# Optimization experiments

Hardware: AMD Instinct MI355X
Metric: run time of the kernel (lower is better)

## Reference

```python
import jax, jax.numpy as jnp
import numpy as np

IN_F, OUT_F = 1024, 1024
GRID_SIZE, SPLINE_ORDER = 5, 3
BATCH = 4096


def _make_grid():
    # grid_range = [-1, 1], h = 2 / grid_size
    h = 2.0 / GRID_SIZE
    g = jnp.arange(-SPLINE_ORDER, GRID_SIZE + SPLINE_ORDER + 1, dtype=jnp.float32) * h - 1.0
    return jnp.broadcast_to(g, (IN_F, g.shape[0]))  # [in, 12]


def setup_inputs() -> dict:
    key = jax.random.key(0)
    k1, k2, k3, k4 = jax.random.split(key, 4)
    x = jax.random.normal(k1, (BATCH, IN_F), dtype=jnp.float32) * 0.5
    base_weight = jax.random.normal(k2, (OUT_F, IN_F), dtype=jnp.float32) * (1.0 / np.sqrt(IN_F))
    # matches reset_parameters noise scale: (rand-0.5)*0.1/grid_size
    spline_weight = (jax.random.uniform(k3, (OUT_F, IN_F, GRID_SIZE + SPLINE_ORDER)) - 0.5) * (0.1 / GRID_SIZE)
    spline_scaler = jax.random.normal(k4, (OUT_F, IN_F), dtype=jnp.float32) * (1.0 / np.sqrt(IN_F))
    return {"x": x, "base_weight": base_weight, "spline_weight": spline_weight,
            "spline_scaler": spline_scaler, "grid": _make_grid()}


def _b_splines(x, grid):
    # x: [B, F], grid: [F, G]; returns [B, F, grid_size + spline_order]
    xe = x[..., None]  # [B, F, 1]
    bases = ((xe >= grid[:, :-1]) & (xe < grid[:, 1:])).astype(x.dtype)  # [B,F,G-1]
    for k in range(1, SPLINE_ORDER + 1):
        left = (xe - grid[:, : -(k + 1)]) / (grid[:, k:-1] - grid[:, : -(k + 1)])
        right = (grid[:, k + 1 :] - xe) / (grid[:, k + 1 :] - grid[:, 1:-k])
        bases = left * bases[:, :, :-1] + right * bases[:, :, 1:]
    return bases


def reference(x, base_weight, spline_weight, spline_scaler, grid):
    base_out = jax.nn.silu(x) @ base_weight.T  # [B, out]
    basis = _b_splines(x, grid)  # [B, in, 8]
    scaled_w = spline_weight * spline_scaler[..., None]  # [out, in, 8]
    spline_out = jnp.einsum('bfi,ofi->bo', basis, scaled_w)
    return base_out + spline_out
```

## Files before the change

### kernel.cpp

```cpp
#include <hip/hip_runtime.h>
#include <hip/hip_bf16.h>

#define IN_F   1024
#define OUT_F  1024
#define GS     5
#define SO     3
#define NB     (GS + SO)
#define NG     (GS + 2*SO + 1)
#define BATCH  4096
#define KC     (IN_F + IN_F * NB)
#define BM 128
#define BN 128
#define BK 64
#define SPLITK 2
#define KPART  (KC / SPLITK)
#define NT     (KPART / BK)

typedef __bf16 bf16x8 __attribute__((ext_vector_type(8)));
typedef float  f32x4  __attribute__((ext_vector_type(4)));

__device__ __forceinline__ void gload_lds16(const void* g, void* l) {
    __builtin_amdgcn_global_load_lds(
        (const __attribute__((address_space(1))) void*)g,
        (__attribute__((address_space(3))) void*)l,
        16, 0, 0);
}

#define WC_BLK 4608
#define A_BLK  18432

__global__ __launch_bounds__(256) void prep_all(const float* __restrict__ bw,
                                                const float* __restrict__ sw,
                                                const float* __restrict__ ss,
                                                const float* __restrict__ x,
                                                __bf16* __restrict__ W,
                                                __bf16* __restrict__ A) {
    if (blockIdx.x < WC_BLK) {
        const int t = blockIdx.x * 256 + threadIdx.x;
        const int NBASE = OUT_F * IN_F / 8;
        if (t < NBASE) {
            const int o  = t >> 7;
            const int c8 = (t & 127) * 8;
            const float4* sp = (const float4*)(bw + (size_t)o * IN_F + c8);
            float4 v0 = sp[0], v1 = sp[1];
            float v[8] = {v0.x, v0.y, v0.z, v0.w, v1.x, v1.y, v1.z, v1.w};
            bf16x8 ov;
#pragma unroll
            for (int j = 0; j < 8; ++j) ov[j] = (__bf16)v[j];
            *(bf16x8*)(W + (size_t)o * KC + c8) = ov;
        } else {
            const int u = t - NBASE;
            if (u >= OUT_F * IN_F) return;
            const int o = u >> 10, f = u & 1023;
            const float s = ss[(size_t)o * IN_F + f];
            const float4* sp = (const float4*)(sw + ((size_t)o * IN_F + f) * NB);
            float4 v0 = sp[0], v1 = sp[1];
            float v[8] = {v0.x, v0.y, v0.z, v0.w, v1.x, v1.y, v1.z, v1.w};
            bf16x8 ov;
#pragma unroll
            for (int j = 0; j < 8; ++j) ov[j] = (__bf16)(v[j] * s);
            *(bf16x8*)(W + (size_t)o * KC + IN_F + (size_t)f * NB) = ov;
        }
    } else {
        const int t = (blockIdx.x - WC_BLK) * 256 + threadIdx.x;
        const int NBASE = BATCH * IN_F / 8;
        if (t < NBASE) {
            const int b  = t >> 7;
            const int c8 = (t & 127) * 8;
            const float4* sp = (const float4*)(x + (size_t)b * IN_F + c8);
            float4 v0 = sp[0], v1 = sp[1];
            float v[8] = {v0.x, v0.y, v0.z, v0.w, v1.x, v1.y, v1.z, v1.w};
            bf16x8 ov;
#pragma unroll
            for (int j = 0; j < 8; ++j) {
                float xx = v[j];
                ov[j] = (__bf16)(xx / (1.0f + __expf(-xx)));
            }
            *(bf16x8*)(A + (size_t)b * KC + c8) = ov;
        } else {
            const int u = t - NBASE;
            if (u >= BATCH * IN_F) return;
            const int b = u >> 10, f = u & 1023;
            const float xv = x[(size_t)b * IN_F + f];
            const float h = 2.0f / GS;
            float gv[NG];
#pragma unroll
            for (int j = 0; j < NG; ++j) gv[j] = (float)(j - SO) * h - 1.0f;
            float bas[NB + SO];
#pragma unroll
            for (int j = 0; j < NB + SO; ++j)
                bas[j] = (xv >= gv[j] && xv < gv[j + 1]) ? 1.0f : 0.0f;
#pragma unroll
            for (int k = 1; k <= SO; ++k) {
                const float rk = 1.0f / ((float)k * h);
#pragma unroll
                for (int j = 0; j <= (NB + SO - 1) - k; ++j) {
                    float left  = (xv - gv[j]) * rk;
                    float right = (gv[j + k + 1] - xv) * rk;
                    bas[j] = left * bas[j] + right * bas[j + 1];
                }
            }
            bf16x8 ov;
#pragma unroll
            for (int i = 0; i < NB; ++i) ov[i] = (__bf16)bas[i];
            *(bf16x8*)(A + (size_t)b * KC + IN_F + (size_t)f * NB) = ov;
        }
    }
}

__global__ __launch_bounds__(256) void zero_out(float4* __restrict__ p, int n4) {
    const int i = blockIdx.x * 256 + threadIdx.x;
    if (i < n4) p[i] = float4{0.f, 0.f, 0.f, 0.f};
}

__global__ __launch_bounds__(256) void reduce_k(float4* __restrict__ C,
                                                const float4* __restrict__ P) {
    const size_t n4 = (size_t)BATCH * OUT_F / 4;
    for (size_t i = blockIdx.x * 256 + threadIdx.x; i < n4; i += 2048 * 256) {
        float4 c = C[i], p = P[i];
        c.x += p.x; c.y += p.y; c.z += p.z; c.w += p.w;
        C[i] = c;
    }
}

#define MFMA_Q(AF, BF, NI0)                                                   \
    __builtin_amdgcn_s_setprio(1);                                            \
    _Pragma("unroll")                                                         \
    for (int kk_ = 0; kk_ < 2; ++kk_)                                         \
        _Pragma("unroll")                                                     \
        for (int i_ = 0; i_ < 4; ++i_)                                        \
            _Pragma("unroll")                                                 \
            for (int n_ = 0; n_ < 2; ++n_)                                    \
                acc[i_][(NI0) + n_] =                                         \
                    __builtin_amdgcn_mfma_f32_16x16x32_bf16(                  \
                        AF[i_][kk_], BF[n_][kk_], acc[i_][(NI0) + n_],        \
                        0, 0, 0);                                             \
    __builtin_amdgcn_s_setprio(0);

#define LGKM0_FENCE do {                                                      \
    asm volatile("s_waitcnt lgkmcnt(0)" ::: "memory");                        \
    __builtin_amdgcn_sched_barrier(0); } while (0)

template<bool ATOMIC>
__global__ __launch_bounds__(256, 2) void kan_gemm(const __bf16* __restrict__ A,
                                                   const __bf16* __restrict__ W,
                                                   float* __restrict__ C,
                                                   float* __restrict__ P) {
    __shared__ __bf16 sA[2][BM * BK];
    __shared__ __bf16 sB[2][BN * BK];

    const int tid  = threadIdx.x;
    const int gid  = blockIdx.x;
    const int work = (gid & 7) * 64 + (gid >> 3);
    const int ks = work >> 8;
    const int bn = (work >> 5) & 7;
    const int bm = work & 31;

    const int lane = tid & 63;
    const int wv   = tid >> 6;
    const int wm   = wv >> 1;
    const int wn   = wv & 1;
    const int lr   = lane & 15;
    const int hi   = lane >> 4;
    const int key  = lr & 7;

    const int slot0 = ((hi ^ key) << 3);
    const int slot1 = (((4 + hi) ^ key) << 3);
    const int aBase = (wm * 64 + lr) * BK;
    const int bBase = (wn * 64 + lr) * BK;

    const __bf16* gA = A + (size_t)(bm * BM) * KC + ks * KPART;
    const __bf16* gW = W + (size_t)(bn * BN) * KC + ks * KPART;

    f32x4 acc[4][4] = {};
    bf16x8 af[4][2], bf01[2][2], bf23[2][2];

    auto stage = [&](int buf, int kt) {
#pragma unroll
        for (int p = 0; p < 4; ++p) {
            const int chunk = p * 256 + tid;
            const int row = chunk >> 3, slot = chunk & 7;
            const int col = (slot ^ (row & 7)) << 3;
            gload_lds16(gA + (size_t)row * KC + kt * BK + col,
                        &sA[buf][chunk * 8]);
        }
#pragma unroll
        for (int p = 0; p < 4; ++p) {
            const int chunk = p * 256 + tid;
            const int row = chunk >> 3, slot = chunk & 7;
            const int col = (slot ^ (row & 7)) << 3;
            gload_lds16(gW + (size_t)row * KC + kt * BK + col,
                        &sB[buf][chunk * 8]);
        }
    };

    stage(0, 0);
    asm volatile("s_waitcnt vmcnt(0)\n\ts_barrier" ::: "memory");

    for (int kt = 0; kt < NT; ++kt) {
        const int b = kt & 1;
        const __bf16* LA = &sA[b][0];
        const __bf16* LB = &sB[b][0];

#pragma unroll
        for (int i_ = 0; i_ < 4; ++i_) {
            af[i_][0] = *(const bf16x8*)&LA[aBase + i_ * (16 * BK) + slot0];
            af[i_][1] = *(const bf16x8*)&LA[aBase + i_ * (16 * BK) + slot1];
        }
#pragma unroll
        for (int n_ = 0; n_ < 2; ++n_) {
            bf01[n_][0] = *(const bf16x8*)&LB[bBase + n_ * (16 * BK) + slot0];
            bf01[n_][1] = *(const bf16x8*)&LB[bBase + n_ * (16 * BK) + slot1];
        }
        if (kt + 1 < NT) stage(b ^ 1, kt + 1);
        LGKM0_FENCE;
        MFMA_Q(af, bf01, 0);

#pragma unroll
        for (int n_ = 0; n_ < 2; ++n_) {
            bf23[n_][0] = *(const bf16x8*)&LB[bBase + (n_ + 2) * (16 * BK) + slot0];
            bf23[n_][1] = *(const bf16x8*)&LB[bBase + (n_ + 2) * (16 * BK) + slot1];
        }
        LGKM0_FENCE;
        MFMA_Q(af, bf23, 2);

        if (kt + 1 < NT)
            asm volatile("s_waitcnt vmcnt(0)\n\ts_barrier" ::: "memory");
    }

    const int cr = hi * 4, cc = lane & 15;
    float* dst;
    if (ATOMIC) dst = C;
    else        dst = (ks == 0) ? C : P;
#pragma unroll
    for (int mi = 0; mi < 4; ++mi)
#pragma unroll
        for (int ni = 0; ni < 4; ++ni) {
            float* cp = dst + (size_t)(bm * BM + wm * 64 + mi * 16 + cr) * OUT_F
                            + bn * BN + wn * 64 + ni * 16 + cc;
#pragma unroll
            for (int r = 0; r < 4; ++r) {
                if (ATOMIC) unsafeAtomicAdd(cp + (size_t)r * OUT_F, acc[mi][ni][r]);
                else        cp[(size_t)r * OUT_F] = acc[mi][ni][r];
            }
        }
}

extern "C" void kernel_launch(void* const* d_in, const int* in_sizes, int n_in,
                              void* d_out, int out_size, void* d_ws, size_t ws_size,
                              hipStream_t stream) {
    const float* x    = (const float*)d_in[0];
    const float* bw   = (const float*)d_in[1];
    const float* sw   = (const float*)d_in[2];
    const float* ss   = (const float*)d_in[3];

    const size_t wc_bytes   = (size_t)OUT_F * KC * 2;
    const size_t a_bytes    = (size_t)BATCH * KC * 2;
    const size_t part_bytes = (size_t)BATCH * OUT_F * 4;
    if (ws_size < wc_bytes + a_bytes) return;

    __bf16* Wc = (__bf16*)d_ws;
    __bf16* A  = (__bf16*)((char*)d_ws + wc_bytes);
    float*  P  = (float*)((char*)d_ws + wc_bytes + a_bytes);

    prep_all<<<WC_BLK + A_BLK, 256, 0, stream>>>(bw, ss ? sw : sw, ss, x, Wc, A);

    const int grid = (BATCH / BM) * (OUT_F / BN) * SPLITK;
    if (ws_size >= wc_bytes + a_bytes + part_bytes) {
        kan_gemm<false><<<grid, 256, 0, stream>>>(A, Wc, (float*)d_out, P);
        reduce_k<<<2048, 256, 0, stream>>>((float4*)d_out, (const float4*)P);
    } else {
        const int n4 = BATCH * OUT_F / 4;
        zero_out<<<n4 / 256, 256, 0, stream>>>((float4*)d_out, n4);
        kan_gemm<true><<<grid, 256, 0, stream>>>(A, Wc, (float*)d_out, P);
    }
}
```

Baseline: 117.5 us.

## Load A fragments directly from global into registers, bypassing LDS

The A operand is no longer staged through shared memory. Each wave now loads its A fragments straight from global memory into registers and double-buffers them across tiles (aC/aN), while B keeps its LDS double buffer. All four B column blocks are read at once, and a single 32-MFMA block replaces the two 16-MFMA halves, with the loop unrolled by two. This halves LDS traffic and footprint, but the A reads from global are strided per lane and less coalesced, and register pressure rises.

```diff
diff --git a/kernel.cpp b/kernel.cpp
--- a/kernel.cpp
+++ b/kernel.cpp
@@ -123,30 +123,52 @@
     }
 }
 
-#define MFMA_Q(AF, BF, NI0)                                                   \
+#define LOAD_A(DST, KT)                                                       \
+    _Pragma("unroll")                                                         \
+    for (int m_ = 0; m_ < 4; ++m_) {                                          \
+        DST[m_][0] = *(const bf16x8*)&aRowPtr[(size_t)m_ * 16 * KC + (KT) * BK];      \
+        DST[m_][1] = *(const bf16x8*)&aRowPtr[(size_t)m_ * 16 * KC + (KT) * BK + 32]; \
+    }
+
+#define READ_B(DST, BUF)                                                      \
+    _Pragma("unroll")                                                         \
+    for (int n_ = 0; n_ < 4; ++n_) {                                          \
+        DST[n_][0] = *(const bf16x8*)&sB[BUF][bBase + n_ * 1024 + slot0];     \
+        DST[n_][1] = *(const bf16x8*)&sB[BUF][bBase + n_ * 1024 + slot1];     \
+    }
+
+#define MFMA32(AF, BF)                                                        \
     __builtin_amdgcn_s_setprio(1);                                            \
     _Pragma("unroll")                                                         \
     for (int kk_ = 0; kk_ < 2; ++kk_)                                         \
         _Pragma("unroll")                                                     \
-        for (int i_ = 0; i_ < 4; ++i_)                                        \
+        for (int m_ = 0; m_ < 4; ++m_)                                        \
             _Pragma("unroll")                                                 \
-            for (int n_ = 0; n_ < 2; ++n_)                                    \
-                acc[i_][(NI0) + n_] =                                         \
-                    __builtin_amdgcn_mfma_f32_16x16x32_bf16(                  \
-                        AF[i_][kk_], BF[n_][kk_], acc[i_][(NI0) + n_],        \
-                        0, 0, 0);                                             \
+            for (int n_ = 0; n_ < 4; ++n_)                                    \
+                acc[m_][n_] = __builtin_amdgcn_mfma_f32_16x16x32_bf16(        \
+                    AF[m_][kk_], BF[n_][kk_], acc[m_][n_], 0, 0, 0);          \
     __builtin_amdgcn_s_setprio(0);
 
-#define LGKM0_FENCE do {                                                      \
-    asm volatile("s_waitcnt lgkmcnt(0)" ::: "memory");                        \
-    __builtin_amdgcn_sched_barrier(0); } while (0)
+#define TILE(KT, BUF, ACUR, ANXT)                                             \
+    do {                                                                      \
+        if ((KT) + 1 < NT) {                                                  \
+            stage((BUF) ^ 1, (KT) + 1);             \
+            LOAD_A(ANXT, (KT) + 1);                      \
+        }                                                                     \
+        __builtin_amdgcn_sched_barrier(0);         \
+        READ_B(bfr, BUF);                                                     \
+        asm volatile("s_waitcnt lgkmcnt(0)" ::: "memory");                    \
+        __builtin_amdgcn_sched_barrier(0);                                    \
+        MFMA32(ACUR, bfr);                                                    \
+        if ((KT) + 1 < NT)                                                    \
+            asm volatile("s_waitcnt vmcnt(0)\n\ts_barrier" ::: "memory");     \
+    } while (0)
 
 template<bool ATOMIC>
 __global__ __launch_bounds__(256, 2) void kan_gemm(const __bf16* __restrict__ A,
                                                    const __bf16* __restrict__ W,
                                                    float* __restrict__ C,
                                                    float* __restrict__ P) {
-    __shared__ __bf16 sA[2][BM * BK];
     __shared__ __bf16 sB[2][BN * BK];
 
     const int tid  = threadIdx.x;
@@ -166,24 +188,16 @@
 
     const int slot0 = ((hi ^ key) << 3);
     const int slot1 = (((4 + hi) ^ key) << 3);
-    const int aBase = (wm * 64 + lr) * BK;
     const int bBase = (wn * 64 + lr) * BK;
 
     const __bf16* gA = A + (size_t)(bm * BM) * KC + ks * KPART;
     const __bf16* gW = W + (size_t)(bn * BN) * KC + ks * KPART;
+    const __bf16* aRowPtr = gA + (size_t)(wm * 64 + lr) * KC + hi * 8;
 
     f32x4 acc[4][4] = {};
-    bf16x8 af[4][2], bf01[2][2], bf23[2][2];
+    bf16x8 aC[4][2], aN[4][2], bfr[4][2];
 
     auto stage = [&](int buf, int kt) {
-#pragma unroll
-        for (int p = 0; p < 4; ++p) {
-            const int chunk = p * 256 + tid;
-            const int row = chunk >> 3, slot = chunk & 7;
-            const int col = (slot ^ (row & 7)) << 3;
-            gload_lds16(gA + (size_t)row * KC + kt * BK + col,
-                        &sA[buf][chunk * 8]);
-        }
 #pragma unroll
         for (int p = 0; p < 4; ++p) {
             const int chunk = p * 256 + tid;
@@ -195,37 +209,12 @@
     };
 
     stage(0, 0);
+    LOAD_A(aC, 0);
     asm volatile("s_waitcnt vmcnt(0)\n\ts_barrier" ::: "memory");
 
-    for (int kt = 0; kt < NT; ++kt) {
-        const int b = kt & 1;
-        const __bf16* LA = &sA[b][0];
-        const __bf16* LB = &sB[b][0];
-
-#pragma unroll
-        for (int i_ = 0; i_ < 4; ++i_) {
-            af[i_][0] = *(const bf16x8*)&LA[aBase + i_ * (16 * BK) + slot0];
-            af[i_][1] = *(const bf16x8*)&LA[aBase + i_ * (16 * BK) + slot1];
-        }
-#pragma unroll
-        for (int n_ = 0; n_ < 2; ++n_) {
-            bf01[n_][0] = *(const bf16x8*)&LB[bBase + n_ * (16 * BK) + slot0];
-            bf01[n_][1] = *(const bf16x8*)&LB[bBase + n_ * (16 * BK) + slot1];
-        }
-        if (kt + 1 < NT) stage(b ^ 1, kt + 1);
-        LGKM0_FENCE;
-        MFMA_Q(af, bf01, 0);
-
-#pragma unroll
-        for (int n_ = 0; n_ < 2; ++n_) {
-            bf23[n_][0] = *(const bf16x8*)&LB[bBase + (n_ + 2) * (16 * BK) + slot0];
-            bf23[n_][1] = *(const bf16x8*)&LB[bBase + (n_ + 2) * (16 * BK) + slot1];
-        }
-        LGKM0_FENCE;
-        MFMA_Q(af, bf23, 2);
-
-        if (kt + 1 < NT)
-            asm volatile("s_waitcnt vmcnt(0)\n\ts_barrier" ::: "memory");
+    for (int kt = 0; kt < NT; kt += 2) {
+        TILE(kt,     0, aC, aN);
+        TILE(kt + 1, 1, aN, aC);
     }
 
     const int cr = hi * 4, cc = lane & 15;
@@ -263,7 +252,7 @@
     __bf16* A  = (__bf16*)((char*)d_ws + wc_bytes);
     float*  P  = (float*)((char*)d_ws + wc_bytes + a_bytes);
 
-    prep_all<<<WC_BLK + A_BLK, 256, 0, stream>>>(bw, ss ? sw : sw, ss, x, Wc, A);
+    prep_all<<<WC_BLK + A_BLK, 256, 0, stream>>>(bw, sw, ss, x, Wc, A);
 
     const int grid = (BATCH / BM) * (OUT_F / BN) * SPLITK;
     if (ws_size >= wc_bytes + a_bytes + part_bytes) {
```

After: 205.6 us. +74.9%, slower.

## Retile GEMM to 128x256 tiles with 512 threads, BK32 and split-K of four

Applied to the files above, without the earlier changes.

Widens the output tile to 128x256 using 8 waves per block, halves the K step to 32 with a matching 4-slot swizzle, and raises split-K from 2 to 4. Grid size stays at 512 blocks. The LDS fragment loads now overlap the first MFMA group through a partial lgkmcnt wait. The reduction kernel now reads three partial buffers, which triples the partial workspace and the extra global traffic, in exchange for more reuse of A per block and more waves in flight.

```diff
diff --git a/kernel.cpp b/kernel.cpp
--- a/kernel.cpp
+++ b/kernel.cpp
@@ -10,9 +10,9 @@
 #define BATCH  4096
 #define KC     (IN_F + IN_F * NB)
 #define BM 128
-#define BN 128
-#define BK 64
-#define SPLITK 2
+#define BN 256
+#define BK 32
+#define SPLITK 4
 #define KPART  (KC / SPLITK)
 #define NT     (KPART / BK)
 
@@ -117,32 +117,36 @@
                                                 const float4* __restrict__ P) {
     const size_t n4 = (size_t)BATCH * OUT_F / 4;
     for (size_t i = blockIdx.x * 256 + threadIdx.x; i < n4; i += 2048 * 256) {
-        float4 c = C[i], p = P[i];
-        c.x += p.x; c.y += p.y; c.z += p.z; c.w += p.w;
+        float4 c  = C[i];
+        float4 p0 = P[i];
+        float4 p1 = P[n4 + i];
+        float4 p2 = P[2 * n4 + i];
+        c.x += p0.x + p1.x + p2.x;
+        c.y += p0.y + p1.y + p2.y;
+        c.z += p0.z + p1.z + p2.z;
+        c.w += p0.w + p1.w + p2.w;
         C[i] = c;
     }
 }
 
-#define MFMA_Q(AF, BF, NI0)                                                   \
+#define SB0 __builtin_amdgcn_sched_barrier(0)
+
+#define LGKM_FENCE(N)                                                         \
+    asm volatile("s_waitcnt lgkmcnt(" #N ")" ::: "memory");                   \
+    __builtin_amdgcn_sched_barrier(0)
+
+#define MFMAQ(BF, NI0)                                                        \
     __builtin_amdgcn_s_setprio(1);                                            \
     _Pragma("unroll")                                                         \
-    for (int kk_ = 0; kk_ < 2; ++kk_)                                         \
+    for (int mt_ = 0; mt_ < 4; ++mt_)                                         \
         _Pragma("unroll")                                                     \
-        for (int i_ = 0; i_ < 4; ++i_)                                        \
-            _Pragma("unroll")                                                 \
-            for (int n_ = 0; n_ < 2; ++n_)                                    \
-                acc[i_][(NI0) + n_] =                                         \
-                    __builtin_amdgcn_mfma_f32_16x16x32_bf16(                  \
-                        AF[i_][kk_], BF[n_][kk_], acc[i_][(NI0) + n_],        \
-                        0, 0, 0);                                             \
+        for (int n_ = 0; n_ < 2; ++n_)                                        \
+            acc[mt_][(NI0) + n_] = __builtin_amdgcn_mfma_f32_16x16x32_bf16(   \
+                af[mt_], BF[n_], acc[mt_][(NI0) + n_], 0, 0, 0);              \
     __builtin_amdgcn_s_setprio(0);
 
-#define LGKM0_FENCE do {                                                      \
-    asm volatile("s_waitcnt lgkmcnt(0)" ::: "memory");                        \
-    __builtin_amdgcn_sched_barrier(0); } while (0)
-
 template<bool ATOMIC>
-__global__ __launch_bounds__(256, 2) void kan_gemm(const __bf16* __restrict__ A,
+__global__ __launch_bounds__(512, 4) void kan_gemm(const __bf16* __restrict__ A,
                                                    const __bf16* __restrict__ W,
                                                    float* __restrict__ C,
                                                    float* __restrict__ P) {
@@ -152,43 +156,40 @@
     const int tid  = threadIdx.x;
     const int gid  = blockIdx.x;
     const int work = (gid & 7) * 64 + (gid >> 3);
-    const int ks = work >> 8;
-    const int bn = (work >> 5) & 7;
+    const int ks = work >> 7;
+    const int bn = (work >> 5) & 3;
     const int bm = work & 31;
 
     const int lane = tid & 63;
     const int wv   = tid >> 6;
-    const int wm   = wv >> 1;
-    const int wn   = wv & 1;
+    const int wm   = wv >> 2;
+    const int wn   = wv & 3;
     const int lr   = lane & 15;
     const int hi   = lane >> 4;
-    const int key  = lr & 7;
-
-    const int slot0 = ((hi ^ key) << 3);
-    const int slot1 = (((4 + hi) ^ key) << 3);
-    const int aBase = (wm * 64 + lr) * BK;
-    const int bBase = (wn * 64 + lr) * BK;
+    const int key  = (lr >> 1) & 3;
+
+    const int slotRd = (hi ^ key) << 3;
+    const int aBase  = (wm * 64 + lr) * BK;
+    const int bBase  = (wn * 64 + lr) * BK;
 
     const __bf16* gA = A + (size_t)(bm * BM) * KC + ks * KPART;
     const __bf16* gW = W + (size_t)(bn * BN) * KC + ks * KPART;
 
     f32x4 acc[4][4] = {};
-    bf16x8 af[4][2], bf01[2][2], bf23[2][2];
+    bf16x8 af[4], b01[2], b23[2];
 
     auto stage = [&](int buf, int kt) {
-#pragma unroll
-        for (int p = 0; p < 4; ++p) {
-            const int chunk = p * 256 + tid;
-            const int row = chunk >> 3, slot = chunk & 7;
-            const int col = (slot ^ (row & 7)) << 3;
+        {
+            const int row = tid >> 2, slot = tid & 3;
+            const int col = (slot ^ ((row >> 1) & 3)) << 3;
             gload_lds16(gA + (size_t)row * KC + kt * BK + col,
-                        &sA[buf][chunk * 8]);
-        }
-#pragma unroll
-        for (int p = 0; p < 4; ++p) {
-            const int chunk = p * 256 + tid;
-            const int row = chunk >> 3, slot = chunk & 7;
-            const int col = (slot ^ (row & 7)) << 3;
+                        &sA[buf][tid * 8]);
+        }
+#pragma unroll
+        for (int l = 0; l < 2; ++l) {
+            const int chunk = l * 512 + tid;
+            const int row = chunk >> 2, slot = chunk & 3;
+            const int col = (slot ^ ((row >> 1) & 3)) << 3;
             gload_lds16(gW + (size_t)row * KC + kt * BK + col,
                         &sB[buf][chunk * 8]);
         }
@@ -202,27 +203,24 @@
         const __bf16* LA = &sA[b][0];
         const __bf16* LB = &sB[b][0];
 
-#pragma unroll
-        for (int i_ = 0; i_ < 4; ++i_) {
-            af[i_][0] = *(const bf16x8*)&LA[aBase + i_ * (16 * BK) + slot0];
-            af[i_][1] = *(const bf16x8*)&LA[aBase + i_ * (16 * BK) + slot1];
-        }
-#pragma unroll
-        for (int n_ = 0; n_ < 2; ++n_) {
-            bf01[n_][0] = *(const bf16x8*)&LB[bBase + n_ * (16 * BK) + slot0];
-            bf01[n_][1] = *(const bf16x8*)&LB[bBase + n_ * (16 * BK) + slot1];
-        }
         if (kt + 1 < NT) stage(b ^ 1, kt + 1);
-        LGKM0_FENCE;
-        MFMA_Q(af, bf01, 0);
-
-#pragma unroll
-        for (int n_ = 0; n_ < 2; ++n_) {
-            bf23[n_][0] = *(const bf16x8*)&LB[bBase + (n_ + 2) * (16 * BK) + slot0];
-            bf23[n_][1] = *(const bf16x8*)&LB[bBase + (n_ + 2) * (16 * BK) + slot1];
-        }
-        LGKM0_FENCE;
-        MFMA_Q(af, bf23, 2);
+
+#pragma unroll
+        for (int mt_ = 0; mt_ < 4; ++mt_)
+            af[mt_] = *(const bf16x8*)&LA[aBase + mt_ * 512 + slotRd];
+#pragma unroll
+        for (int n_ = 0; n_ < 2; ++n_)
+            b01[n_] = *(const bf16x8*)&LB[bBase + n_ * 512 + slotRd];
+        SB0;
+#pragma unroll
+        for (int n_ = 0; n_ < 2; ++n_)
+            b23[n_] = *(const bf16x8*)&LB[bBase + (2 + n_) * 512 + slotRd];
+
+        LGKM_FENCE(2);
+        MFMAQ(b01, 0);
+
+        LGKM_FENCE(0);
+        MFMAQ(b23, 2);
 
         if (kt + 1 < NT)
             asm volatile("s_waitcnt vmcnt(0)\n\ts_barrier" ::: "memory");
@@ -231,17 +229,17 @@
     const int cr = hi * 4, cc = lane & 15;
     float* dst;
     if (ATOMIC) dst = C;
-    else        dst = (ks == 0) ? C : P;
-#pragma unroll
-    for (int mi = 0; mi < 4; ++mi)
-#pragma unroll
-        for (int ni = 0; ni < 4; ++ni) {
-            float* cp = dst + (size_t)(bm * BM + wm * 64 + mi * 16 + cr) * OUT_F
-                            + bn * BN + wn * 64 + ni * 16 + cc;
+    else        dst = (ks == 0) ? C : P + (size_t)(ks - 1) * BATCH * OUT_F;
+#pragma unroll
+    for (int mt = 0; mt < 4; ++mt)
+#pragma unroll
+        for (int nt = 0; nt < 4; ++nt) {
+            float* cp = dst + (size_t)(bm * BM + wm * 64 + mt * 16 + cr) * OUT_F
+                            + bn * BN + wn * 64 + nt * 16 + cc;
 #pragma unroll
             for (int r = 0; r < 4; ++r) {
-                if (ATOMIC) unsafeAtomicAdd(cp + (size_t)r * OUT_F, acc[mi][ni][r]);
-                else        cp[(size_t)r * OUT_F] = acc[mi][ni][r];
+                if (ATOMIC) unsafeAtomicAdd(cp + (size_t)r * OUT_F, acc[mt][nt][r]);
+                else        cp[(size_t)r * OUT_F] = acc[mt][nt][r];
             }
         }
 }
@@ -256,22 +254,22 @@
 
     const size_t wc_bytes   = (size_t)OUT_F * KC * 2;
     const size_t a_bytes    = (size_t)BATCH * KC * 2;
-    const size_t part_bytes = (size_t)BATCH * OUT_F * 4;
+    const size_t part_bytes = 3ull * BATCH * OUT_F * 4;
     if (ws_size < wc_bytes + a_bytes) return;
 
     __bf16* Wc = (__bf16*)d_ws;
     __bf16* A  = (__bf16*)((char*)d_ws + wc_bytes);
     float*  P  = (float*)((char*)d_ws + wc_bytes + a_bytes);
 
-    prep_all<<<WC_BLK + A_BLK, 256, 0, stream>>>(bw, ss ? sw : sw, ss, x, Wc, A);
+    prep_all<<<WC_BLK + A_BLK, 256, 0, stream>>>(bw, sw, ss, x, Wc, A);
 
     const int grid = (BATCH / BM) * (OUT_F / BN) * SPLITK;
     if (ws_size >= wc_bytes + a_bytes + part_bytes) {
-        kan_gemm<false><<<grid, 256, 0, stream>>>(A, Wc, (float*)d_out, P);
+        kan_gemm<false><<<grid, 512, 0, stream>>>(A, Wc, (float*)d_out, P);
         reduce_k<<<2048, 256, 0, stream>>>((float4*)d_out, (const float4*)P);
     } else {
         const int n4 = BATCH * OUT_F / 4;
         zero_out<<<n4 / 256, 256, 0, stream>>>((float4*)d_out, n4);
-        kan_gemm<true><<<grid, 256, 0, stream>>>(A, Wc, (float*)d_out, P);
-    }
-}
+        kan_gemm<true><<<grid, 512, 0, stream>>>(A, Wc, (float*)d_out, P);
+    }
+}
```

After: 127.2 us. 1.08x slower.
